# Kernel optimization log

Hardware: AMD Instinct MI355X
Metric: run time of the kernel (lower is better)

The kernel has to match this reference:

```python
import jax, jax.numpy as jnp
import numpy as np

N_NODES = 100000
N_EDGES = 1600000
F_IN, HIDDEN, N_CLASS = 64, 48, 40


def setup_inputs() -> dict:
    key = jax.random.key(0)
    ks = jax.random.split(key, 9)
    def glorot(k, fi, fo):
        s = (6.0 / (fi + fo)) ** 0.5
        return jax.random.uniform(k, (fi, fo), jnp.float32, -s, s)
    return {
        "x": jax.random.normal(ks[0], (N_NODES, F_IN), jnp.float32),
        "edge_index": jax.random.randint(ks[1], (2, N_EDGES), 0, N_NODES, jnp.int64),
        "edge_weight": jax.random.uniform(ks[2], (N_EDGES,), jnp.float32),
        "W1": glorot(ks[3], F_IN, HIDDEN),   # ARMAConv init_weight (K=1)
        "V1": glorot(ks[4], F_IN, HIDDEN),   # ARMAConv root_weight
        "b1": jnp.zeros((HIDDEN,), jnp.float32),
        "W2": glorot(ks[5], HIDDEN, N_CLASS),
        "V2": glorot(ks[6], HIDDEN, N_CLASS),
        "b2": jnp.zeros((N_CLASS,), jnp.float32),
    }


def _arma_conv(x, W, V, b, src, dst, norm, num_nodes):
    # out = ReLU( A_norm @ (x @ W) + x @ V + b )   (num_stacks=1, num_layers=1)
    h = x @ W                                   # [N, F_out]
    msg = h[src] * norm[:, None]                # gather + scale  [E, F_out]
    agg = jax.ops.segment_sum(msg, dst, num_segments=num_nodes)  # scatter-add
    return jax.nn.relu(agg + x @ V + b)


def reference(x, edge_index, edge_weight, W1, V1, b1, W2, V2, b2):
    num_nodes = x.shape[0]
    src, dst = edge_index[0], edge_index[1]
    # gcn_norm, add_self_loops=False: D^{-1/2} A D^{-1/2}
    deg = jax.ops.segment_sum(edge_weight, dst, num_segments=num_nodes)
    dinv = jnp.where(deg > 0, jax.lax.rsqrt(jnp.where(deg > 0, deg, 1.0)), 0.0)
    norm = dinv[src] * edge_weight * dinv[dst]
    # eval mode: input dropout is identity
    h = _arma_conv(x, W1, V1, b1, src, dst, norm, num_nodes)
    h = _arma_conv(h, W2, V2, b2, src, dst, norm, num_nodes)
    return jax.nn.log_softmax(h, axis=-1)
```

## Files before the change

kernel.cpp:

```cpp
#include <hip/hip_runtime.h>
#include <math.h>


constexpr int F_IN = 64;
constexpr int HIDDEN = 48;
constexpr int N_CLASS = 40;
constexpr int CHUNK = 8192;
constexpr int BIN_SHIFT = 9;
constexpr int BIN_CAP = 9216;
constexpr int CSR_CAP = 12288;

typedef __attribute__((ext_vector_type(8))) short bf16x8;
typedef __attribute__((ext_vector_type(4))) float f32x4;

__device__ __forceinline__ short bfr(float f) {
    unsigned u = __float_as_uint(f);
    return (short)((u + 0x7fffu + ((u >> 16) & 1u)) >> 16);
}
__device__ __forceinline__ unsigned pack_bf2(float a, float b) {
    unsigned ua = __float_as_uint(a), ub = __float_as_uint(b);
    ua = (ua + 0x7fffu + ((ua >> 16) & 1u)) >> 16;
    ub = (ub + 0x7fffu + ((ub >> 16) & 1u)) >> 16;
    return ua | (ub << 16);
}
__device__ __forceinline__ float2 unpack_bf2(unsigned u) {
    return make_float2(__uint_as_float(u << 16), __uint_as_float(u & 0xffff0000u));
}
__device__ __forceinline__ bf16x8 cvt8(float4 f0, float4 f1) {
    bf16x8 r;
    r[0] = bfr(f0.x); r[1] = bfr(f0.y); r[2] = bfr(f0.z); r[3] = bfr(f0.w);
    r[4] = bfr(f1.x); r[5] = bfr(f1.y); r[6] = bfr(f1.z); r[7] = bfr(f1.w);
    return r;
}

__global__ void init_cursor(int* __restrict__ binCursor) {
    binCursor[threadIdx.x] = (int)threadIdx.x * BIN_CAP;
}

__global__ __launch_bounds__(256) void gemm1_kernel(
    const float* __restrict__ X, const float* __restrict__ W,
    const float* __restrict__ V, const float* __restrict__ b,
    unsigned* __restrict__ XWp, unsigned* __restrict__ AGGp, int N) {
    __shared__ char smem[36864];
    short* sWT = (short*)smem;
    float* ep = (float*)(smem + 12288);
    int tid = threadIdx.x;
    for (int i = tid; i < 96 * 64; i += 256) {
        int c = i >> 6, k = i & 63;
        float v = (c < 48) ? W[k * 48 + c] : V[k * 48 + (c - 48)];
        sWT[i] = bfr(v);
    }
    __syncthreads();

    int lane = tid & 63, wv = tid >> 6;
    int m = lane & 15, quad = lane >> 4;
    int nb0 = (int)blockIdx.x * 64;
    int n = nb0 + wv * 16 + m;

    bf16x8 a0, a1;
    if (n < N) {
        const float4* xr = (const float4*)(X + (size_t)n * 64 + quad * 8);
        a0 = cvt8(xr[0], xr[1]);
        const float4* xr2 = (const float4*)(X + (size_t)n * 64 + 32 + quad * 8);
        a1 = cvt8(xr2[0], xr2[1]);
    } else {
        for (int j = 0; j < 8; ++j) { a0[j] = 0; a1[j] = 0; }
    }

    f32x4 acc[6];
#pragma unroll
    for (int ct = 0; ct < 6; ++ct) acc[ct] = (f32x4){0.f, 0.f, 0.f, 0.f};
#pragma unroll
    for (int ct = 0; ct < 6; ++ct) {
        bf16x8 b0 = *(const bf16x8*)(sWT + (ct * 16 + m) * 64 + quad * 8);
        bf16x8 b1 = *(const bf16x8*)(sWT + (ct * 16 + m) * 64 + 32 + quad * 8);
        acc[ct] = __builtin_amdgcn_mfma_f32_16x16x32_bf16(a0, b0, acc[ct], 0, 0, 0);
        acc[ct] = __builtin_amdgcn_mfma_f32_16x16x32_bf16(a1, b1, acc[ct], 0, 0, 0);
    }
#pragma unroll
    for (int ct = 0; ct < 6; ++ct)
#pragma unroll
        for (int r = 0; r < 4; ++r)
            ep[(wv * 16 + quad * 4 + r) * 96 + ct * 16 + m] = acc[ct][r];
    __syncthreads();
    for (int i = tid; i < 64 * 24; i += 256) {
        int r = i / 24, c2 = i - r * 24;
        int node = nb0 + r;
        if (node >= N) continue;
        float w0 = ep[r * 96 + 2 * c2], w1 = ep[r * 96 + 2 * c2 + 1];
        XWp[node * 24 + c2] = pack_bf2(w0, w1);
        float v0 = ep[r * 96 + 48 + 2 * c2], v1 = ep[r * 96 + 48 + 2 * c2 + 1];
        float2 bb = ((const float2*)b)[c2];
        AGGp[node * 24 + c2] = pack_bf2(v0 + bb.x, v1 + bb.y);
    }
}

__global__ __launch_bounds__(256) void binscatter(
    const int* __restrict__ src, const int* __restrict__ dst,
    const float* __restrict__ w, int* __restrict__ binCursor,
    int2* __restrict__ binned, int E) {
    __shared__ int sx[CHUNK];
    __shared__ int sw[CHUNK];
    __shared__ unsigned char sbin[CHUNK];
    __shared__ int hist[256];
    int tid = threadIdx.x;
    hist[tid] = 0;
    __syncthreads();
    long long e0 = (long long)blockIdx.x * CHUNK;
    int M = (int)min((long long)CHUNK, (long long)E - e0);
    for (int i = tid; i < M; i += 256) {
        int d = dst[e0 + i];
        int bn = d >> BIN_SHIFT;
        sx[i] = ((d & 511) << 17) | src[e0 + i];
        sw[i] = __float_as_int(w[e0 + i]);
        sbin[i] = (unsigned char)bn;
        atomicAdd(&hist[bn], 1);
    }
    __syncthreads();
    int base = atomicAdd(&binCursor[tid], hist[tid]);
    __syncthreads();
    hist[tid] = base;
    __syncthreads();
    for (int i = tid; i < M; i += 256) {
        int p = atomicAdd(&hist[sbin[i]], 1);
        binned[p] = make_int2(sx[i], sw[i]);
    }
}

__global__ __launch_bounds__(512) void build_csr(const int2* __restrict__ binned,
                                                 const int* __restrict__ binCursor,
                                                 int* __restrict__ rowBeg,
                                                 int* __restrict__ rowEnd,
                                                 float* __restrict__ dinv,
                                                 unsigned* __restrict__ csr,
                                                 unsigned* __restrict__ XW1p, int N) {
    __shared__ int sx[CSR_CAP];
    __shared__ int sw[CSR_CAP];
    __shared__ int cntL[512];
    __shared__ float degL[512];
    __shared__ int scanL[512];
    int b = blockIdx.x, tid = threadIdx.x;
    int e0 = b * BIN_CAP;
    int M = min(binCursor[b] - e0, BIN_CAP);
    cntL[tid] = 0;
    degL[tid] = 0.f;
    __syncthreads();
    for (int i = tid; i < M; i += 512) {
        int2 p = binned[e0 + i];
        sx[i] = p.x;
        sw[i] = p.y;
        int dl = ((unsigned)p.x) >> 17;
        atomicAdd(&cntL[dl], 1);
        atomicAdd(&degL[dl], __int_as_float(p.y));
    }
    __syncthreads();
    int v = cntL[tid];
    scanL[tid] = v;
    __syncthreads();
#pragma unroll
    for (int o = 1; o < 512; o <<= 1) {
        int u = (tid >= o) ? scanL[tid - o] : 0;
        __syncthreads();
        scanL[tid] += u;
        __syncthreads();
    }
    int excl = scanL[tid] - v;
    int node = (b << BIN_SHIFT) + tid;
    float dg = degL[tid];
    float dv = dg > 0.f ? rsqrtf(dg) : 0.f;
    if (node < N) {
        rowBeg[node] = e0 + excl;
        rowEnd[node] = e0 + excl + v;
        dinv[node] = dv;
    }
    cntL[tid] = e0 + excl;
    degL[tid] = dv;
    __syncthreads();
    for (int i = tid; i < M; i += 512) {
        int px = sx[i], pw = sw[i];
        int dl = ((unsigned)px) >> 17;
        int pos = atomicAdd(&cntL[dl], 1);
        float wn = __int_as_float(pw) * degL[dl];
        unsigned uw = __float_as_uint(wn);
        uw = (uw + 0x7fffu + ((uw >> 16) & 1u)) >> 16;
        csr[pos] = ((unsigned)(px & 0x1FFFF) << 15) | uw;
    }
    int nb0 = b << BIN_SHIFT;
    for (int i = tid; i < 512 * 24; i += 512) {
        int nl = i / 24, c = i - nl * 24;
        int nn = nb0 + nl;
        if (nn >= N) break;
        float dvn = degL[nl];
        float2 u = unpack_bf2(XW1p[nn * 24 + c]);
        XW1p[nn * 24 + c] = pack_bf2(u.x * dvn, u.y * dvn);
    }
}

template <int W>
__device__ __forceinline__ void edge4(const unsigned* __restrict__ XWp, uint4 p4,
                                      int c, float4& s) {
    uint2 u0 = *(const uint2*)(XWp + (p4.x >> 15) * W + c);
    uint2 u1 = *(const uint2*)(XWp + (p4.y >> 15) * W + c);
    uint2 u2 = *(const uint2*)(XWp + (p4.z >> 15) * W + c);
    uint2 u3 = *(const uint2*)(XWp + (p4.w >> 15) * W + c);
    float n0 = __uint_as_float((p4.x & 0x7FFFu) << 16);
    float n1 = __uint_as_float((p4.y & 0x7FFFu) << 16);
    float n2 = __uint_as_float((p4.z & 0x7FFFu) << 16);
    float n3 = __uint_as_float((p4.w & 0x7FFFu) << 16);
    float2 a0 = unpack_bf2(u0.x), b0 = unpack_bf2(u0.y);
    float2 a1 = unpack_bf2(u1.x), b1 = unpack_bf2(u1.y);
    float2 a2 = unpack_bf2(u2.x), b2 = unpack_bf2(u2.y);
    float2 a3 = unpack_bf2(u3.x), b3 = unpack_bf2(u3.y);
    s.x = fmaf(a0.x, n0, s.x); s.y = fmaf(a0.y, n0, s.y);
    s.z = fmaf(b0.x, n0, s.z); s.w = fmaf(b0.y, n0, s.w);
    s.x = fmaf(a1.x, n1, s.x); s.y = fmaf(a1.y, n1, s.y);
    s.z = fmaf(b1.x, n1, s.z); s.w = fmaf(b1.y, n1, s.w);
    s.x = fmaf(a2.x, n2, s.x); s.y = fmaf(a2.y, n2, s.y);
    s.z = fmaf(b2.x, n2, s.z); s.w = fmaf(b2.y, n2, s.w);
    s.x = fmaf(a3.x, n3, s.x); s.y = fmaf(a3.y, n3, s.y);
    s.z = fmaf(b3.x, n3, s.z); s.w = fmaf(b3.y, n3, s.w);
}

template <int W>
__device__ __forceinline__ float4 row_accum2(const unsigned* __restrict__ XWp,
                                             const unsigned* __restrict__ csr,
                                             int j, int end, int c, float4 s) {
    while (j < end && (j & 3)) {
        unsigned p = csr[j++];
        uint2 u = *(const uint2*)(XWp + (p >> 15) * W + c);
        float nr = __uint_as_float((p & 0x7FFFu) << 16);
        float2 x0 = unpack_bf2(u.x), x1 = unpack_bf2(u.y);
        s.x = fmaf(x0.x, nr, s.x); s.y = fmaf(x0.y, nr, s.y);
        s.z = fmaf(x1.x, nr, s.z); s.w = fmaf(x1.y, nr, s.w);
    }
    int nch = (end - j) >> 2;
    if (nch > 0) {
        uint4 p4 = *(const uint4*)(csr + j);
        for (int k = 1; k < nch; ++k) {
            uint4 p4n = *(const uint4*)(csr + j + (k << 2));
            edge4<W>(XWp, p4, c, s);
            p4 = p4n;
        }
        edge4<W>(XWp, p4, c, s);
        j += nch << 2;
    }
    for (; j < end; ++j) {
        unsigned p = csr[j];
        uint2 u = *(const uint2*)(XWp + (p >> 15) * W + c);
        float nr = __uint_as_float((p & 0x7FFFu) << 16);
        float2 x0 = unpack_bf2(u.x), x1 = unpack_bf2(u.y);
        s.x = fmaf(x0.x, nr, s.x); s.y = fmaf(x0.y, nr, s.y);
        s.z = fmaf(x1.x, nr, s.z); s.w = fmaf(x1.y, nr, s.w);
    }
    return s;
}

__global__ __launch_bounds__(384) void pull_agg(const unsigned* __restrict__ XWp,
                                                const unsigned* __restrict__ csr,
                                                const int* __restrict__ rowBeg,
                                                const int* __restrict__ rowEnd,
                                                const unsigned* __restrict__ AGG1p,
                                                unsigned* __restrict__ H1p, int N) {
    int t = blockIdx.x * blockDim.x + threadIdx.x;
    int n = t / 12, c1 = t - n * 12;
    if (n >= N) return;
    int c = 2 * c1;
    uint2 a = *(const uint2*)(AGG1p + n * 24 + c);
    float2 f0 = unpack_bf2(a.x), f1 = unpack_bf2(a.y);
    float4 s = make_float4(f0.x, f0.y, f1.x, f1.y);
    s = row_accum2<24>(XWp, csr, rowBeg[n], rowEnd[n], c, s);
    uint2 o;
    o.x = pack_bf2(fmaxf(s.x, 0.f), fmaxf(s.y, 0.f));
    o.y = pack_bf2(fmaxf(s.z, 0.f), fmaxf(s.w, 0.f));
    *(uint2*)(H1p + n * 24 + c) = o;
}

__global__ __launch_bounds__(256) void gemm2_kernel(
    const short* __restrict__ H1, const float* __restrict__ W,
    const float* __restrict__ V, const float* __restrict__ b,
    const float* __restrict__ dinv, unsigned* __restrict__ XWp,
    unsigned* __restrict__ AGGp, int N) {
    __shared__ char smem[30720];
    short* sWT = (short*)smem;
    float* ep = (float*)(smem + 10240);
    int tid = threadIdx.x;
    for (int i = tid; i < 80 * 64; i += 256) {
        int c = i >> 6, k = i & 63;
        float v = 0.f;
        if (k < 48) v = (c < 40) ? W[k * 40 + c] : V[k * 40 + (c - 40)];
        sWT[i] = bfr(v);
    }
    __syncthreads();

    int lane = tid & 63, wv = tid >> 6;
    int m = lane & 15, quad = lane >> 4;
    int nb0 = (int)blockIdx.x * 64;
    int n = nb0 + wv * 16 + m;

    bf16x8 a0, a1;
    if (n < N) {
        a0 = *(const bf16x8*)(H1 + (size_t)n * 48 + quad * 8);
        if (quad < 2) {
            a1 = *(const bf16x8*)(H1 + (size_t)n * 48 + 32 + quad * 8);
        } else {
            for (int j = 0; j < 8; ++j) a1[j] = 0;
        }
    } else {
        for (int j = 0; j < 8; ++j) { a0[j] = 0; a1[j] = 0; }
    }

    f32x4 acc[5];
#pragma unroll
    for (int ct = 0; ct < 5; ++ct) acc[ct] = (f32x4){0.f, 0.f, 0.f, 0.f};
#pragma unroll
    for (int ct = 0; ct < 5; ++ct) {
        bf16x8 b0 = *(const bf16x8*)(sWT + (ct * 16 + m) * 64 + quad * 8);
        bf16x8 b1 = *(const bf16x8*)(sWT + (ct * 16 + m) * 64 + 32 + quad * 8);
        acc[ct] = __builtin_amdgcn_mfma_f32_16x16x32_bf16(a0, b0, acc[ct], 0, 0, 0);
        acc[ct] = __builtin_amdgcn_mfma_f32_16x16x32_bf16(a1, b1, acc[ct], 0, 0, 0);
    }
#pragma unroll
    for (int ct = 0; ct < 5; ++ct)
#pragma unroll
        for (int r = 0; r < 4; ++r)
            ep[(wv * 16 + quad * 4 + r) * 80 + ct * 16 + m] = acc[ct][r];
    __syncthreads();
    for (int i = tid; i < 64 * 20; i += 256) {
        int r = i / 20, c2 = i - r * 20;
        int node = nb0 + r;
        if (node >= N) continue;
        float dv = dinv[node];
        float w0 = ep[r * 80 + 2 * c2], w1 = ep[r * 80 + 2 * c2 + 1];
        XWp[node * 20 + c2] = pack_bf2(w0 * dv, w1 * dv);
        float v0 = ep[r * 80 + 40 + 2 * c2], v1 = ep[r * 80 + 40 + 2 * c2 + 1];
        float2 bb = ((const float2*)b)[c2];
        AGGp[node * 20 + c2] = pack_bf2(v0 + bb.x, v1 + bb.y);
    }
}

__global__ __launch_bounds__(320) void pull_ls(const unsigned* __restrict__ XWp,
                                               const unsigned* __restrict__ csr,
                                               const int* __restrict__ rowBeg,
                                               const int* __restrict__ rowEnd,
                                               const unsigned* __restrict__ AGG2p,
                                               float* __restrict__ out, int N) {
    __shared__ float4 sbuf[32 * 10];
    __shared__ float sl[32];
    int tid = threadIdx.x;
    int nl = tid / 10, c1 = tid - nl * 10;
    int n = blockIdx.x * 32 + nl;
    int c = 2 * c1;
    float4 s = make_float4(0.f, 0.f, 0.f, 0.f);
    if (n < N) {
        uint2 a = *(const uint2*)(AGG2p + n * 20 + c);
        float2 f0 = unpack_bf2(a.x), f1 = unpack_bf2(a.y);
        s = make_float4(f0.x, f0.y, f1.x, f1.y);
        s = row_accum2<20>(XWp, csr, rowBeg[n], rowEnd[n], c, s);
    }
    sbuf[nl * 10 + c1] = s;
    __syncthreads();
    if (tid < 32) {
        float m = 0.f;
        for (int k = 0; k < 10; ++k) {
            float4 v = sbuf[tid * 10 + k];
            m = fmaxf(m, fmaxf(fmaxf(v.x, v.y), fmaxf(v.z, v.w)));
        }
        float sum = 0.f;
        for (int k = 0; k < 10; ++k) {
            float4 v = sbuf[tid * 10 + k];
            sum += expf(fmaxf(v.x, 0.f) - m) + expf(fmaxf(v.y, 0.f) - m) +
                   expf(fmaxf(v.z, 0.f) - m) + expf(fmaxf(v.w, 0.f) - m);
        }
        sl[tid] = m + logf(sum);
    }
    __syncthreads();
    if (n < N) {
        float l = sl[nl];
        ((float4*)out)[n * 10 + c1] =
            make_float4(fmaxf(s.x, 0.f) - l, fmaxf(s.y, 0.f) - l,
                        fmaxf(s.z, 0.f) - l, fmaxf(s.w, 0.f) - l);
    }
}

extern "C" void kernel_launch(void* const* d_in, const int* in_sizes, int n_in,
                              void* d_out, int out_size, void* d_ws, size_t ws_size,
                              hipStream_t stream) {
    const float* x  = (const float*)d_in[0];
    const int*   ei = (const int*)d_in[1];
    const float* ew = (const float*)d_in[2];
    const float* W1 = (const float*)d_in[3];
    const float* V1 = (const float*)d_in[4];
    const float* b1 = (const float*)d_in[5];
    const float* W2 = (const float*)d_in[6];
    const float* V2 = (const float*)d_in[7];
    const float* b2 = (const float*)d_in[8];
    float* out = (float*)d_out;

    const int N = in_sizes[0] / F_IN;
    const int E = in_sizes[2];
    const int* src = ei;
    const int* dst = ei + E;

    char* ws = (char*)d_ws;
    size_t off = 0;
    auto carve = [&](size_t bytes) {
        void* p = ws + off;
        off = (off + bytes + 255) & ~size_t(255);
        return p;
    };
    int*      binCursor = (int*)carve(256 * 4);
    int*      rowBeg    = (int*)carve((size_t)N * 4);
    int*      rowEnd    = (int*)carve((size_t)N * 4);
    float*    dinv      = (float*)carve((size_t)N * 4);
    int2*     binned    = (int2*)carve((size_t)256 * BIN_CAP * 8);
    unsigned* csr       = (unsigned*)carve((size_t)256 * BIN_CAP * 4);
    unsigned* xW1p      = (unsigned*)carve((size_t)N * 24 * 4);
    unsigned* agg1p     = (unsigned*)carve((size_t)N * 24 * 4);
    unsigned* h1p       = (unsigned*)carve((size_t)N * 24 * 4);
    unsigned* xW2p      = (unsigned*)carve((size_t)N * 20 * 4);
    unsigned* agg2p     = (unsigned*)carve((size_t)N * 20 * 4);

    const int B = 256;
    auto cdiv = [](long long a, long long b) { return (int)((a + b - 1) / b); };
    const int nSc = cdiv(E, CHUNK);
    const int nBins = (N + (1 << BIN_SHIFT) - 1) >> BIN_SHIFT;
    const int nGemmBlocks = cdiv(N, 64);

    init_cursor<<<1, 256, 0, stream>>>(binCursor);
    binscatter<<<nSc, B, 0, stream>>>(src, dst, ew, binCursor, binned, E);
    gemm1_kernel<<<nGemmBlocks, B, 0, stream>>>(x, W1, V1, b1, xW1p, agg1p, N);
    build_csr<<<nBins, 512, 0, stream>>>(binned, binCursor, rowBeg, rowEnd,
                                         dinv, csr, xW1p, N);

    pull_agg<<<cdiv((long long)N * 12, 384), 384, 0, stream>>>(xW1p, csr, rowBeg,
                                                               rowEnd, agg1p, h1p, N);

    gemm2_kernel<<<nGemmBlocks, B, 0, stream>>>((const short*)h1p, W2, V2, b2,
                                                dinv, xW2p, agg2p, N);

    pull_ls<<<cdiv(N, 32), 320, 0, stream>>>(xW2p, csr, rowBeg, rowEnd,
                                             agg2p, out, N);
}
```

Before: 269.5 us.

## Use finer CSR bins with register-staged edge binning and smaller CSR blocks

Shrinks destination bins from 512 to 128 nodes and the scatter chunk from 8192 to 2048 edges, giving several times more blocks to both the binning and the CSR-build kernels. The binning kernel keeps its edges in registers instead of shared-memory staging arrays. The CSR-build kernel now uses 256 threads and re-reads binned edges from global memory instead of caching them in shared memory. The aim is to fill the GPU with more and lighter blocks and cut shared-memory pressure during CSR construction. The cost is many more global cursor atomics, less coalesced scatter writes, since each bin receives only a few edges per chunk, and a second global read of the binned edges.

Result: slower. 277.5 us (+2.9%).

```diff
diff --git a/kernel.cpp b/kernel.cpp
--- a/kernel.cpp
+++ b/kernel.cpp
@@ -5,10 +5,11 @@
 constexpr int F_IN = 64;
 constexpr int HIDDEN = 48;
 constexpr int N_CLASS = 40;
-constexpr int CHUNK = 8192;
-constexpr int BIN_SHIFT = 9;
-constexpr int BIN_CAP = 9216;
-constexpr int CSR_CAP = 12288;
+constexpr int CHUNK = 2048;
+constexpr int EPT = CHUNK / 256;
+constexpr int BIN_SHIFT = 7;
+constexpr int BIN_CAP = 2560;
+constexpr int MAXBINS = 1024;
 
 typedef __attribute__((ext_vector_type(8))) short bf16x8;
 typedef __attribute__((ext_vector_type(4))) float f32x4;
@@ -98,95 +99,98 @@
 __global__ __launch_bounds__(256) void binscatter(
     const int* __restrict__ src, const int* __restrict__ dst,
     const float* __restrict__ w, int* __restrict__ binCursor,
-    int2* __restrict__ binned, int E) {
-    __shared__ int sx[CHUNK];
-    __shared__ int sw[CHUNK];
-    __shared__ unsigned char sbin[CHUNK];
-    __shared__ int hist[256];
+    int2* __restrict__ binned, int E, int NB) {
+    __shared__ int hist[MAXBINS];
     int tid = threadIdx.x;
-    hist[tid] = 0;
+    for (int j = tid; j < NB; j += 256) hist[j] = 0;
     __syncthreads();
     long long e0 = (long long)blockIdx.x * CHUNK;
     int M = (int)min((long long)CHUNK, (long long)E - e0);
-    for (int i = tid; i < M; i += 256) {
-        int d = dst[e0 + i];
-        int bn = d >> BIN_SHIFT;
-        sx[i] = ((d & 511) << 17) | src[e0 + i];
-        sw[i] = __float_as_int(w[e0 + i]);
-        sbin[i] = (unsigned char)bn;
-        atomicAdd(&hist[bn], 1);
-    }
-    __syncthreads();
-    int base = atomicAdd(&binCursor[tid], hist[tid]);
-    __syncthreads();
-    hist[tid] = base;
-    __syncthreads();
-    for (int i = tid; i < M; i += 256) {
-        int p = atomicAdd(&hist[sbin[i]], 1);
-        binned[p] = make_int2(sx[i], sw[i]);
-    }
-}
-
-__global__ __launch_bounds__(512) void build_csr(const int2* __restrict__ binned,
+    int dv[EPT], sv[EPT], wv[EPT];
+#pragma unroll
+    for (int q = 0; q < EPT; ++q) {
+        int i = tid + q * 256;
+        if (i < M) {
+            dv[q] = dst[e0 + i];
+            sv[q] = src[e0 + i];
+            wv[q] = __float_as_int(w[e0 + i]);
+            atomicAdd(&hist[dv[q] >> BIN_SHIFT], 1);
+        }
+    }
+    __syncthreads();
+    for (int j = tid; j < NB; j += 256) {
+        int h = hist[j];
+        hist[j] = h ? atomicAdd(&binCursor[j], h) : 0;
+    }
+    __syncthreads();
+#pragma unroll
+    for (int q = 0; q < EPT; ++q) {
+        int i = tid + q * 256;
+        if (i < M) {
+            int d = dv[q];
+            int p = atomicAdd(&hist[d >> BIN_SHIFT], 1);
+            binned[p] = make_int2(((d & (BIN_CAP - 1) & 127) << 17) | sv[q], wv[q]);
+        }
+    }
+}
+
+__global__ __launch_bounds__(256) void build_csr(const int2* __restrict__ binned,
                                                  const int* __restrict__ binCursor,
                                                  int* __restrict__ rowBeg,
                                                  int* __restrict__ rowEnd,
                                                  float* __restrict__ dinv,
                                                  unsigned* __restrict__ csr,
                                                  unsigned* __restrict__ XW1p, int N) {
-    __shared__ int sx[CSR_CAP];
-    __shared__ int sw[CSR_CAP];
-    __shared__ int cntL[512];
-    __shared__ float degL[512];
-    __shared__ int scanL[512];
+    __shared__ int cntL[128];
+    __shared__ float degL[128];
+    __shared__ int scanL[128];
     int b = blockIdx.x, tid = threadIdx.x;
     int e0 = b * BIN_CAP;
     int M = min(binCursor[b] - e0, BIN_CAP);
-    cntL[tid] = 0;
-    degL[tid] = 0.f;
-    __syncthreads();
-    for (int i = tid; i < M; i += 512) {
+    if (tid < 128) { cntL[tid] = 0; degL[tid] = 0.f; }
+    __syncthreads();
+    for (int i = tid; i < M; i += 256) {
         int2 p = binned[e0 + i];
-        sx[i] = p.x;
-        sw[i] = p.y;
         int dl = ((unsigned)p.x) >> 17;
         atomicAdd(&cntL[dl], 1);
         atomicAdd(&degL[dl], __int_as_float(p.y));
     }
     __syncthreads();
-    int v = cntL[tid];
-    scanL[tid] = v;
-    __syncthreads();
-#pragma unroll
-    for (int o = 1; o < 512; o <<= 1) {
-        int u = (tid >= o) ? scanL[tid - o] : 0;
+    int v = 0;
+    if (tid < 128) { v = cntL[tid]; scanL[tid] = v; }
+    __syncthreads();
+#pragma unroll
+    for (int o = 1; o < 128; o <<= 1) {
+        int u = (tid < 128 && tid >= o) ? scanL[tid - o] : 0;
         __syncthreads();
-        scanL[tid] += u;
+        if (tid < 128) scanL[tid] += u;
         __syncthreads();
     }
-    int excl = scanL[tid] - v;
-    int node = (b << BIN_SHIFT) + tid;
-    float dg = degL[tid];
-    float dv = dg > 0.f ? rsqrtf(dg) : 0.f;
-    if (node < N) {
-        rowBeg[node] = e0 + excl;
-        rowEnd[node] = e0 + excl + v;
-        dinv[node] = dv;
-    }
-    cntL[tid] = e0 + excl;
-    degL[tid] = dv;
-    __syncthreads();
-    for (int i = tid; i < M; i += 512) {
-        int px = sx[i], pw = sw[i];
-        int dl = ((unsigned)px) >> 17;
+    if (tid < 128) {
+        int excl = scanL[tid] - v;
+        int node = (b << BIN_SHIFT) + tid;
+        float dg = degL[tid];
+        float dvv = dg > 0.f ? rsqrtf(dg) : 0.f;
+        if (node < N) {
+            rowBeg[node] = e0 + excl;
+            rowEnd[node] = e0 + excl + v;
+            dinv[node] = dvv;
+        }
+        cntL[tid] = e0 + excl;
+        degL[tid] = dvv;
+    }
+    __syncthreads();
+    for (int i = tid; i < M; i += 256) {
+        int2 p = binned[e0 + i];
+        int dl = ((unsigned)p.x) >> 17;
         int pos = atomicAdd(&cntL[dl], 1);
-        float wn = __int_as_float(pw) * degL[dl];
+        float wn = __int_as_float(p.y) * degL[dl];
         unsigned uw = __float_as_uint(wn);
         uw = (uw + 0x7fffu + ((uw >> 16) & 1u)) >> 16;
-        csr[pos] = ((unsigned)(px & 0x1FFFF) << 15) | uw;
+        csr[pos] = ((unsigned)(p.x & 0x1FFFF) << 15) | uw;
     }
     int nb0 = b << BIN_SHIFT;
-    for (int i = tid; i < 512 * 24; i += 512) {
+    for (int i = tid; i < 128 * 24; i += 256) {
         int nl = i / 24, c = i - nl * 24;
         int nn = nb0 + nl;
         if (nn >= N) break;
@@ -408,12 +412,15 @@
         off = (off + bytes + 255) & ~size_t(255);
         return p;
     };
-    int*      binCursor = (int*)carve(256 * 4);
+    auto cdiv = [](long long a, long long b) { return (int)((a + b - 1) / b); };
+    const int nBins = cdiv(N, 1 << BIN_SHIFT);
+
+    int*      binCursor = (int*)carve(MAXBINS * 4);
     int*      rowBeg    = (int*)carve((size_t)N * 4);
     int*      rowEnd    = (int*)carve((size_t)N * 4);
     float*    dinv      = (float*)carve((size_t)N * 4);
-    int2*     binned    = (int2*)carve((size_t)256 * BIN_CAP * 8);
-    unsigned* csr       = (unsigned*)carve((size_t)256 * BIN_CAP * 4);
+    int2*     binned    = (int2*)carve((size_t)nBins * BIN_CAP * 8);
+    unsigned* csr       = (unsigned*)carve((size_t)nBins * BIN_CAP * 4);
     unsigned* xW1p      = (unsigned*)carve((size_t)N * 24 * 4);
     unsigned* agg1p     = (unsigned*)carve((size_t)N * 24 * 4);
     unsigned* h1p       = (unsigned*)carve((size_t)N * 24 * 4);
@@ -421,15 +428,13 @@
     unsigned* agg2p     = (unsigned*)carve((size_t)N * 20 * 4);
 
     const int B = 256;
-    auto cdiv = [](long long a, long long b) { return (int)((a + b - 1) / b); };
     const int nSc = cdiv(E, CHUNK);
-    const int nBins = (N + (1 << BIN_SHIFT) - 1) >> BIN_SHIFT;
     const int nGemmBlocks = cdiv(N, 64);
 
-    init_cursor<<<1, 256, 0, stream>>>(binCursor);
-    binscatter<<<nSc, B, 0, stream>>>(src, dst, ew, binCursor, binned, E);
+    init_cursor<<<1, MAXBINS, 0, stream>>>(binCursor);
+    binscatter<<<nSc, B, 0, stream>>>(src, dst, ew, binCursor, binned, E, nBins);
     gemm1_kernel<<<nGemmBlocks, B, 0, stream>>>(x, W1, V1, b1, xW1p, agg1p, N);
-    build_csr<<<nBins, 512, 0, stream>>>(binned, binCursor, rowBeg, rowEnd,
+    build_csr<<<nBins, 256, 0, stream>>>(binned, binCursor, rowBeg, rowEnd,
                                          dinv, csr, xW1p, N);
 
     pull_agg<<<cdiv((long long)N * 12, 384), 384, 0, stream>>>(xW1p, csr, rowBeg,
```

## Fuse edge bin-scatter into gemm1 launch and keep edges in registers

Applied to the files above, without the earlier changes.

Merges the binscatter and gemm1 kernels into one launch, with block-index ranges splitting into edge-binning blocks and GEMM blocks so the two independent stages can run concurrently. The chunk size is halved and each thread now holds its edges in registers instead of staging them in large shared arrays. Global cursor atomics are skipped for empty histogram bins. Costs include more binscatter blocks and more global atomics, and higher register pressure from the per-thread edge arrays.

Measured after the change: 255.4 us. -5.2%, faster.

```diff
diff --git a/kernel.cpp b/kernel.cpp
--- a/kernel.cpp
+++ b/kernel.cpp
@@ -5,7 +5,8 @@
 constexpr int F_IN = 64;
 constexpr int HIDDEN = 48;
 constexpr int N_CLASS = 40;
-constexpr int CHUNK = 8192;
+constexpr int CHUNK = 4096;
+constexpr int EPT = CHUNK / 256;
 constexpr int BIN_SHIFT = 9;
 constexpr int BIN_CAP = 9216;
 constexpr int CSR_CAP = 12288;
@@ -37,14 +38,53 @@
     binCursor[threadIdx.x] = (int)threadIdx.x * BIN_CAP;
 }
 
-__global__ __launch_bounds__(256) void gemm1_kernel(
+__global__ __launch_bounds__(256) void gemm1_binscatter(
     const float* __restrict__ X, const float* __restrict__ W,
     const float* __restrict__ V, const float* __restrict__ b,
-    unsigned* __restrict__ XWp, unsigned* __restrict__ AGGp, int N) {
+    unsigned* __restrict__ XWp, unsigned* __restrict__ AGGp, int N,
+    const int* __restrict__ src, const int* __restrict__ dst,
+    const float* __restrict__ w, int* __restrict__ binCursor,
+    int2* __restrict__ binned, int E, int nSc) {
     __shared__ char smem[36864];
+    int tid = threadIdx.x;
+
+    if ((int)blockIdx.x < nSc) {
+        int* hist = (int*)smem;
+        hist[tid] = 0;
+        __syncthreads();
+        long long e0 = (long long)blockIdx.x * CHUNK;
+        int M = (int)min((long long)CHUNK, (long long)E - e0);
+        int dv[EPT], sv[EPT], wv[EPT];
+#pragma unroll
+        for (int q = 0; q < EPT; ++q) {
+            int i = tid + q * 256;
+            if (i < M) {
+                dv[q] = dst[e0 + i];
+                sv[q] = src[e0 + i];
+                wv[q] = __float_as_int(w[e0 + i]);
+                atomicAdd(&hist[dv[q] >> BIN_SHIFT], 1);
+            }
+        }
+        __syncthreads();
+        int h = hist[tid];
+        int base = h ? atomicAdd(&binCursor[tid], h) : 0;
+        __syncthreads();
+        hist[tid] = base;
+        __syncthreads();
+#pragma unroll
+        for (int q = 0; q < EPT; ++q) {
+            int i = tid + q * 256;
+            if (i < M) {
+                int d = dv[q];
+                int p = atomicAdd(&hist[d >> BIN_SHIFT], 1);
+                binned[p] = make_int2(((d & 511) << 17) | sv[q], wv[q]);
+            }
+        }
+        return;
+    }
+
     short* sWT = (short*)smem;
     float* ep = (float*)(smem + 12288);
-    int tid = threadIdx.x;
     for (int i = tid; i < 96 * 64; i += 256) {
         int c = i >> 6, k = i & 63;
         float v = (c < 48) ? W[k * 48 + c] : V[k * 48 + (c - 48)];
@@ -52,10 +92,10 @@
     }
     __syncthreads();
 
-    int lane = tid & 63, wv = tid >> 6;
+    int lane = tid & 63, wvq = tid >> 6;
     int m = lane & 15, quad = lane >> 4;
-    int nb0 = (int)blockIdx.x * 64;
-    int n = nb0 + wv * 16 + m;
+    int nb0 = ((int)blockIdx.x - nSc) * 64;
+    int n = nb0 + wvq * 16 + m;
 
     bf16x8 a0, a1;
     if (n < N) {
@@ -81,7 +121,7 @@
     for (int ct = 0; ct < 6; ++ct)
 #pragma unroll
         for (int r = 0; r < 4; ++r)
-            ep[(wv * 16 + quad * 4 + r) * 96 + ct * 16 + m] = acc[ct][r];
+            ep[(wvq * 16 + quad * 4 + r) * 96 + ct * 16 + m] = acc[ct][r];
     __syncthreads();
     for (int i = tid; i < 64 * 24; i += 256) {
         int r = i / 24, c2 = i - r * 24;
@@ -92,38 +132,6 @@
         float v0 = ep[r * 96 + 48 + 2 * c2], v1 = ep[r * 96 + 48 + 2 * c2 + 1];
         float2 bb = ((const float2*)b)[c2];
         AGGp[node * 24 + c2] = pack_bf2(v0 + bb.x, v1 + bb.y);
-    }
-}
-
-__global__ __launch_bounds__(256) void binscatter(
-    const int* __restrict__ src, const int* __restrict__ dst,
-    const float* __restrict__ w, int* __restrict__ binCursor,
-    int2* __restrict__ binned, int E) {
-    __shared__ int sx[CHUNK];
-    __shared__ int sw[CHUNK];
-    __shared__ unsigned char sbin[CHUNK];
-    __shared__ int hist[256];
-    int tid = threadIdx.x;
-    hist[tid] = 0;
-    __syncthreads();
-    long long e0 = (long long)blockIdx.x * CHUNK;
-    int M = (int)min((long long)CHUNK, (long long)E - e0);
-    for (int i = tid; i < M; i += 256) {
-        int d = dst[e0 + i];
-        int bn = d >> BIN_SHIFT;
-        sx[i] = ((d & 511) << 17) | src[e0 + i];
-        sw[i] = __float_as_int(w[e0 + i]);
-        sbin[i] = (unsigned char)bn;
-        atomicAdd(&hist[bn], 1);
-    }
-    __syncthreads();
-    int base = atomicAdd(&binCursor[tid], hist[tid]);
-    __syncthreads();
-    hist[tid] = base;
-    __syncthreads();
-    for (int i = tid; i < M; i += 256) {
-        int p = atomicAdd(&hist[sbin[i]], 1);
-        binned[p] = make_int2(sx[i], sw[i]);
     }
 }
 
@@ -427,8 +435,8 @@
     const int nGemmBlocks = cdiv(N, 64);
 
     init_cursor<<<1, 256, 0, stream>>>(binCursor);
-    binscatter<<<nSc, B, 0, stream>>>(src, dst, ew, binCursor, binned, E);
-    gemm1_kernel<<<nGemmBlocks, B, 0, stream>>>(x, W1, V1, b1, xW1p, agg1p, N);
+    gemm1_binscatter<<<nSc + nGemmBlocks, B, 0, stream>>>(
+        x, W1, V1, b1, xW1p, agg1p, N, src, dst, ew, binCursor, binned, E, nSc);
     build_csr<<<nBins, 512, 0, stream>>>(binned, binCursor, rowBeg, rowEnd,
                                          dinv, csr, xW1p, N);
 
```
